# Kernel tuning notes

Measured on AMD Instinct MI355X. Metric: run time of the kernel, lower is better.

The kernel has to match this reference:

```python
import jax, jax.numpy as jnp
import numpy as np

BLOCK_SIZE = 128  # config.block_size; first query block skips intra-block causal mask (faithful to source)
NEG = -1e9       # the module uses -1e9, not -inf, for masking and m_i init


def setup_inputs() -> dict:
    key = jax.random.key(0)
    kq, kk, kv, km = jax.random.split(key, 4)
    B, S, H, D = 2, 2048, 16, 64
    q = jax.random.normal(kq, (B, S, H, D), dtype=jnp.float32)
    k = jax.random.normal(kk, (B, S, H, D), dtype=jnp.float32)
    v = jax.random.normal(kv, (B, S, H, D), dtype=jnp.float32)
    mask = jax.random.randint(km, (B, S), 0, 2).astype(bool)
    mask = mask.at[:, 0].set(True)  # keep first key attendable
    return {"q": q, "k": k, "v": v, "mask": mask}


def reference(q, k, v, mask):
    # q,k,v: [B,S,H,D]; mask: [B,S] bool (True = attend)
    B, S, H, D = q.shape
    scale = 1.0 / np.sqrt(D)
    # config.normalize_query=True -> F.normalize(q, dim=-1) (eps=1e-12)
    qn = q / jnp.maximum(jnp.linalg.norm(q, axis=-1, keepdims=True), 1e-12)
    # scores: [B,S(query),H,S(key)]
    scores = jnp.einsum('bshd,bkhd->bshk', qn, k) * scale
    qi = jnp.arange(S)[:, None]
    ki = jnp.arange(S)[None, :]
    # Faithful causal structure of the blocked PyTorch fallback:
    #  - keys limited to k <= q (triu(diagonal=block_start+1) masking)
    #  - EXCEPT the first query block (block_start==0), where the intra-block
    #    causal mask is skipped (keys still limited to the first block).
    allowed = (ki <= qi) | ((qi < BLOCK_SIZE) & (ki < BLOCK_SIZE))  # [S,S]
    scores = jnp.where(allowed[None, :, None, :], scores, NEG)
    scores = jnp.where(mask[:, None, None, :], scores, NEG)
    p = jax.nn.softmax(scores, axis=-1)
    out = jnp.einsum('bshk,bkhd->bshd', p, v)
    return out
```

## Files before the change

kernel.cpp:

```cpp
#include <hip/hip_runtime.h>
#include <stdint.h>

typedef __attribute__((ext_vector_type(8))) short short8;
typedef __attribute__((ext_vector_type(4))) float floatx4;
typedef __attribute__((ext_vector_type(4))) unsigned int uintx4;
typedef __attribute__((ext_vector_type(2))) unsigned int uintx2;

#define S_LEN 2048
#define NHEAD 16
#define DHEAD 64
#define KB    64
#define KPL   131072
#define VPL   262144
#define VOFF  (32 * KPL)
#define MOFF  (VOFF + 32 * VPL)
#define POFF  (MOFF + 8192)
#define DOFF  (POFF + 512 * 32768)
#define WS_NEEDED ((size_t)DOFF + 512 * 512)
#define NEGINF (-__builtin_inff())
#define LOG2E 1.4426950408889634f
#define CSC   0.011271055f

#define GLOAD_LDS16(gp, lp) \
    __builtin_amdgcn_global_load_lds((const __attribute__((address_space(1))) unsigned int*)(gp), \
                                     (__attribute__((address_space(3))) unsigned int*)(lp), 16, 0, 0)

static __device__ __forceinline__ unsigned f2bf(float f) {
    union { float f; unsigned u; } w; w.f = f;
    return (w.u + 0x7FFFu + ((w.u >> 16) & 1u)) >> 16;
}
static __device__ __forceinline__ unsigned cvtpk(float lo, float hi) {
    unsigned r;
    asm("v_cvt_pk_bf16_f32 %0, %1, %2" : "=v"(r) : "v"(lo), "v"(hi));
    return r;
}
template <int HI>
static __device__ __forceinline__ int cvtfp8(float a, float b, int old) {
    return __builtin_amdgcn_cvt_pk_fp8_f32(a, b, old, HI);
}
static __device__ __forceinline__ floatx4 mfma16(short8 a, short8 b, floatx4 c) {
    return __builtin_amdgcn_mfma_f32_16x16x32_bf16(a, b, c, 0, 0, 0);
}
static __device__ __forceinline__ floatx4 mfma8(long a, long b, floatx4 c) {
    return __builtin_amdgcn_mfma_f32_16x16x32_fp8_fp8(a, b, c, 0, 0, 0);
}

__global__ __launch_bounds__(256) void prep_kernel(
    const float* __restrict__ kg, const float* __restrict__ vg,
    const int* __restrict__ mg, char* __restrict__ ws)
{
    __shared__ unsigned short Tl[64 * 72];
    const int bid = blockIdx.x;
    const int t   = bid & 31;
    const int bh  = bid >> 5;
    const int b   = bh >> 4, h = bh & 15;
    const int tid = threadIdx.x;
    char* kpre = ws + (size_t)bh * KPL;
    char* vpre = ws + VOFF + (size_t)bh * VPL;

    {
        const int r  = tid >> 2;
        const int c4 = tid & 3;
        const size_t grow = (((size_t)b * S_LEN + t * 64 + r) * NHEAD + h) * DHEAD + 16 * c4;
        floatx4 f0 = *(const floatx4*)(kg + grow);
        floatx4 f1 = *(const floatx4*)(kg + grow + 4);
        floatx4 f2 = *(const floatx4*)(kg + grow + 8);
        floatx4 f3 = *(const floatx4*)(kg + grow + 12);
        int w0 = 0, w1 = 0, w2 = 0, w3 = 0;
        w0 = cvtfp8<0>(f0[0], f0[1], w0); w0 = cvtfp8<1>(f0[2], f0[3], w0);
        w1 = cvtfp8<0>(f1[0], f1[1], w1); w1 = cvtfp8<1>(f1[2], f1[3], w1);
        w2 = cvtfp8<0>(f2[0], f2[1], w2); w2 = cvtfp8<1>(f2[2], f2[3], w2);
        w3 = cvtfp8<0>(f3[0], f3[1], w3); w3 = cvtfp8<1>(f3[2], f3[3], w3);
        const int Xr = r & 7;
        char* dst = kpre + t * 4096 + r * 64 + 8 * (((2 * c4) ^ Xr) & ~1);
        *(uintx4*)dst = (Xr & 1)
            ? (uintx4){(unsigned)w2, (unsigned)w3, (unsigned)w0, (unsigned)w1}
            : (uintx4){(unsigned)w0, (unsigned)w1, (unsigned)w2, (unsigned)w3};
    }
    {
        const int key = tid >> 2;
        const int d0  = (tid & 3) * 16;
        const float vz = mg[(size_t)b * S_LEN + t * 64 + key] ? 1.f : 0.f;
        const size_t grow = (((size_t)b * S_LEN + t * 64 + key) * NHEAD + h) * DHEAD;
        #pragma unroll
        for (int q = 0; q < 4; ++q) {
            floatx4 f = *(const floatx4*)(vg + grow + d0 + 4 * q);
            #pragma unroll
            for (int ii = 0; ii < 4; ++ii)
                Tl[(d0 + 4 * q + ii) * 72 + key] = (unsigned short)f2bf(f[ii] * vz);
        }
    }
    __syncthreads();
    {
        const int d  = tid >> 2;
        const int c0 = (tid & 3) * 32;
        const int Xv = (d & 7) << 4;
        #pragma unroll
        for (int cc = 0; cc < 2; ++cc) {
            const int c   = c0 + 16 * cc;
            const int pp0 = (c ^ Xv) >> 1;
            const int blk = pp0 >> 5;
            const int a   = (pp0 & 31) >> 3;
            unsigned short vals[8];
            #pragma unroll
            for (int i = 0; i < 8; ++i) {
                const int key = 32 * blk + ((i < 4) ? (4 * a + i) : (16 + 4 * a + i - 4));
                vals[i] = Tl[d * 72 + key];
            }
            *(uintx4*)(vpre + t * 8192 + d * 128 + c) = *(const uintx4*)vals;
        }
    }
    if (h == 0 && tid < 64) {
        const int key = tid;
        const int gg = (key >> 2) & 3, lo = key & 3;
        const int ks = key >> 5,      hi = (key >> 4) & 1;
        const unsigned short mv = mg[(size_t)b * S_LEN + t * 64 + key] ? 0x3F80 : 0;
        *(unsigned short*)(ws + MOFF + (size_t)b * 4096 + t * 128
                           + gg * 32 + ks * 16 + (4 * hi + lo) * 2) = mv;
    }
}

__global__ __launch_bounds__(512, 4) void fa3_main(
    const float* __restrict__ qg, char* __restrict__ ws,
    float* __restrict__ og)
{
    __shared__ char smem[32768];
    char* Qs  = smem;
    char* KsB = smem + 8192;
    char* VsB = smem + 16384;

    const int tid  = threadIdx.x;
    const int bid  = blockIdx.x;
    const int gidx = bid >> 5;
    const int bh   = bid & 31;
    int qb, chunk; bool split;
    if (gidx < 16) { qb = 15 - (gidx >> 1); chunk = gidx & 1; split = true; }
    else           { qb = 7 - (gidx - 16);  chunk = 0;        split = false; }
    const int b    = bh >> 4;
    const int h    = bh & 15;
    const int w    = tid >> 6;
    const int lane = tid & 63;
    const int g    = lane >> 4;
    const int lm   = lane & 15;
    const int kh   = w >> 2;
    const int wq   = w & 3;
    const char* kpre = ws + (size_t)bh * KPL;
    const char* vpre = ws + VOFF + (size_t)bh * VPL;
    const char* mgf  = ws + MOFF + (size_t)b * 4096;
    const int nkt = (qb == 0) ? 2 : (2 * qb + 2);
    int kt0 = 0, kt1 = nkt;
    if (split) { const int hh = nkt >> 1; kt0 = chunk ? hh : 0; kt1 = chunk ? nkt : hh; }

    if (tid < 256) GLOAD_LDS16(kpre + (size_t)kt0 * 4096 + tid * 16, KsB + tid * 16);
    GLOAD_LDS16(vpre + (size_t)kt0 * 8192 + tid * 16, VsB + tid * 16);

    {
        const int r  = tid >> 2;
        const int q0 = tid & 3;
        const float* src = qg + (((size_t)b * S_LEN + (size_t)qb * 128 + r) * NHEAD + h) * DHEAD + q0 * 16;
        floatx4 f0 = *(const floatx4*)(src + 0);
        floatx4 f1 = *(const floatx4*)(src + 4);
        floatx4 f2 = *(const floatx4*)(src + 8);
        floatx4 f3 = *(const floatx4*)(src + 12);
        float ssq = 0.f;
        #pragma unroll
        for (int i = 0; i < 4; ++i)
            ssq += f0[i]*f0[i] + f1[i]*f1[i] + f2[i]*f2[i] + f3[i]*f3[i];
        ssq += __shfl_xor(ssq, 1);
        ssq += __shfl_xor(ssq, 2);
        const float sc = 16.0f / fmaxf(sqrtf(ssq), 1e-12f);
        int w0 = 0, w1 = 0, w2 = 0, w3 = 0;
        w0 = cvtfp8<0>(f0[0]*sc, f0[1]*sc, w0); w0 = cvtfp8<1>(f0[2]*sc, f0[3]*sc, w0);
        w1 = cvtfp8<0>(f1[0]*sc, f1[1]*sc, w1); w1 = cvtfp8<1>(f1[2]*sc, f1[3]*sc, w1);
        w2 = cvtfp8<0>(f2[0]*sc, f2[1]*sc, w2); w2 = cvtfp8<1>(f2[2]*sc, f2[3]*sc, w2);
        w3 = cvtfp8<0>(f3[0]*sc, f3[1]*sc, w3); w3 = cvtfp8<1>(f3[2]*sc, f3[3]*sc, w3);
        const int Xr = r & 7;
        char* qp = Qs + r * 64 + 8 * (((2 * q0) ^ Xr) & ~1);
        *(uintx4*)qp = (Xr & 1)
            ? (uintx4){(unsigned)w2, (unsigned)w3, (unsigned)w0, (unsigned)w1}
            : (uintx4){(unsigned)w0, (unsigned)w1, (unsigned)w2, (unsigned)w3};
    }
    asm volatile("s_waitcnt vmcnt(0)" ::: "memory");
    __syncthreads();

    const int Xl8  = (lm & 7) << 3;
    const int Xl16 = (lm & 7) << 4;
    long qf8[2][2];
    #pragma unroll
    for (int grp = 0; grp < 2; ++grp) {
        const char* base = Qs + (wq * 32 + grp * 16 + lm) * 64;
        #pragma unroll
        for (int ksd = 0; ksd < 2; ++ksd)
            qf8[grp][ksd] = *(const long*)(base + ((32 * ksd + 8 * g) ^ Xl8));
    }

    floatx4 oacc[2][4];
    floatx4 dacc[2];
    #pragma unroll
    for (int grp = 0; grp < 2; ++grp) {
        dacc[grp] = (floatx4){0.f,0.f,0.f,0.f};
        #pragma unroll
        for (int nt = 0; nt < 4; ++nt) oacc[grp][nt] = (floatx4){0.f,0.f,0.f,0.f};
    }
    floatx4 ZERO4 = (floatx4){0.f,0.f,0.f,0.f};
    asm volatile("" : "+v"(ZERO4));
    const int qgl0 = qb * 128 + wq * 32 + lm;

    int cur = 0;
    for (int kt = kt0; kt < kt1; ++kt) {
        if (kt + 1 < kt1) {
            if (tid < 256)
                GLOAD_LDS16(kpre + (size_t)(kt + 1) * 4096 + tid * 16,
                            KsB + (cur ^ 1) * 4096 + tid * 16);
            GLOAD_LDS16(vpre + (size_t)(kt + 1) * 8192 + tid * 16,
                        VsB + (cur ^ 1) * 8192 + tid * 16);
        }
        const short8 mf = *(const short8*)(mgf + kt * 128 + g * 32 + kh * 16);

        floatx4 st[2][2];
        const char* kbase = KsB + cur * 4096 + kh * 2048 + lm * 64;
        __builtin_amdgcn_s_setprio(1);
        #pragma unroll
        for (int mt = 0; mt < 2; ++mt) {
            long kf = *(const long*)(kbase + mt * 1024 + ((8 * g) ^ Xl8));
            st[0][mt] = mfma8(kf, qf8[0][0], ZERO4);
            st[1][mt] = mfma8(kf, qf8[1][0], ZERO4);
        }
        #pragma unroll
        for (int mt = 0; mt < 2; ++mt) {
            long kf = *(const long*)(kbase + mt * 1024 + ((32 + 8 * g) ^ Xl8));
            st[0][mt] = mfma8(kf, qf8[0][1], st[0][mt]);
            st[1][mt] = mfma8(kf, qf8[1][1], st[1][mt]);
        }
        __builtin_amdgcn_s_setprio(0);

        if ((qb >= 1) && (kt >= 2 * qb)) {
            #pragma unroll
            for (int mt = 0; mt < 2; ++mt)
                #pragma unroll
                for (int j = 0; j < 4; ++j) {
                    const int kgl = kt * KB + kh * 32 + mt * 16 + 4 * g + j;
                    if (kgl > qgl0)      st[0][mt][j] = -1e6f;
                    if (kgl > qgl0 + 16) st[1][mt][j] = -1e6f;
                }
        }

        short8 pa[2];
        #pragma unroll
        for (int grp = 0; grp < 2; ++grp) {
            float p[8];
            #pragma unroll
            for (int mt = 0; mt < 2; ++mt)
                #pragma unroll
                for (int j = 0; j < 4; ++j)
                    p[mt * 4 + j] = exp2f(fmaf(st[grp][mt][j], CSC, -8.0f));
            union { short8 s; uintx4 u; } pu;
            pu.u = (uintx4){ cvtpk(p[0], p[1]), cvtpk(p[2], p[3]),
                             cvtpk(p[4], p[5]), cvtpk(p[6], p[7]) };
            pa[grp] = pu.s;
        }
        __builtin_amdgcn_s_setprio(1);
        dacc[0] = mfma16(pa[0], mf, dacc[0]);
        dacc[1] = mfma16(pa[1], mf, dacc[1]);
        {
            const char* vbase = VsB + cur * 8192 + lm * 128;
            #pragma unroll
            for (int nt = 0; nt < 4; ++nt) {
                short8 vf = *(const short8*)(vbase + nt * 2048 + ((64 * kh + 16 * g) ^ Xl16));
                oacc[0][nt] = mfma16(pa[0], vf, oacc[0][nt]);
                oacc[1][nt] = mfma16(pa[1], vf, oacc[1][nt]);
            }
        }
        __builtin_amdgcn_s_setprio(0);

        asm volatile("s_waitcnt vmcnt(0)" ::: "memory");
        __syncthreads();
        cur ^= 1;
    }

    floatx4* rbuf = (floatx4*)smem;
    float*   dbuf = (float*)smem;
    if (kh == 1) {
        #pragma unroll
        for (int grp = 0; grp < 2; ++grp)
            #pragma unroll
            for (int nt = 0; nt < 4; ++nt)
                rbuf[((grp * 4 + nt) * 4 + wq) * 64 + lane] = oacc[grp][nt];
    }
    __syncthreads();
    if (kh == 0) {
        #pragma unroll
        for (int grp = 0; grp < 2; ++grp)
            #pragma unroll
            for (int nt = 0; nt < 4; ++nt)
                oacc[grp][nt] += rbuf[((grp * 4 + nt) * 4 + wq) * 64 + lane];
    }
    __syncthreads();
    if (kh == 1 && lm == 0) {
        #pragma unroll
        for (int grp = 0; grp < 2; ++grp)
            #pragma unroll
            for (int j = 0; j < 4; ++j)
                dbuf[wq * 32 + grp * 16 + 4 * g + j] = dacc[grp][j];
    }
    __syncthreads();
    if (kh == 0) {
        if (!split) {
            #pragma unroll
            for (int grp = 0; grp < 2; ++grp)
                #pragma unroll
                for (int j = 0; j < 4; ++j) {
                    const int rl = wq * 32 + grp * 16 + 4 * g + j;
                    const float invj = 1.0f / (dacc[grp][j] + dbuf[rl]);
                    float* dst = og + (((size_t)b * S_LEN + qb * 128 + rl) * NHEAD + h) * DHEAD + lm;
                    #pragma unroll
                    for (int nt = 0; nt < 4; ++nt) dst[nt * 16] = oacc[grp][nt][j] * invj;
                }
        } else {
            const int s = ((qb - 8) * 32 + bh) * 2 + chunk;
            float* po = (float*)(ws + POFF + (size_t)s * 32768);
            float* pd = (float*)(ws + DOFF + (size_t)s * 512);
            #pragma unroll
            for (int grp = 0; grp < 2; ++grp)
                #pragma unroll
                for (int j = 0; j < 4; ++j) {
                    const int rl = wq * 32 + grp * 16 + 4 * g + j;
                    #pragma unroll
                    for (int nt = 0; nt < 4; ++nt)
                        po[rl * 64 + nt * 16 + lm] = oacc[grp][nt][j];
                    if (lm == 0) pd[rl] = dacc[grp][j] + dbuf[rl];
                }
        }
    }
}

__global__ __launch_bounds__(256) void fa3_combine(
    const char* __restrict__ ws, float* __restrict__ og)
{
    const int i0  = (blockIdx.x * 256 + threadIdx.x) * 8;
    const int d   = i0 & 63;
    const int row = (i0 >> 6) & 127;
    const int bh  = (i0 >> 13) & 31;
    const int qbi = i0 >> 18;
    const int b   = bh >> 4, h = bh & 15;
    const int s0  = (qbi * 32 + bh) * 2;
    const float* p0 = (const float*)(ws + POFF + (size_t)s0 * 32768) + row * 64 + d;
    const float* p1 = (const float*)(ws + POFF + (size_t)(s0 + 1) * 32768) + row * 64 + d;
    const float den = ((const float*)(ws + DOFF + (size_t)s0 * 512))[row]
                    + ((const float*)(ws + DOFF + (size_t)(s0 + 1) * 512))[row];
    const float inv = 1.0f / den;
    floatx4 a0 = *(const floatx4*)p0, a1 = *(const floatx4*)(p0 + 4);
    floatx4 b0 = *(const floatx4*)p1, b1 = *(const floatx4*)(p1 + 4);
    floatx4 o0, o1;
    #pragma unroll
    for (int i = 0; i < 4; ++i) { o0[i] = (a0[i] + b0[i]) * inv; o1[i] = (a1[i] + b1[i]) * inv; }
    float* dst = og + (((size_t)b * S_LEN + (8 + qbi) * 128 + row) * NHEAD + h) * DHEAD + d;
    *(floatx4*)dst       = o0;
    *(floatx4*)(dst + 4) = o1;
}

__global__ __launch_bounds__(512) void fa3_fallback(
    const float* __restrict__ qg, const float* __restrict__ kg,
    const float* __restrict__ vg, const int* __restrict__ mg,
    float* __restrict__ og)
{
    __shared__ unsigned short Qs[128 * DHEAD];
    __shared__ unsigned short Ks2[KB * DHEAD];
    __shared__ unsigned short Vt[DHEAD * KB];
    __shared__ float Ms[KB];

    const int tid  = threadIdx.x;
    const int bid  = blockIdx.x;
    const int qb   = 15 - (bid >> 5);
    const int bh   = bid & 31;
    const int b    = bh >> 4;
    const int h    = bh & 15;
    const int w    = tid >> 6;
    const int lane = tid & 63;
    const int g    = lane >> 4;
    const int lm   = lane & 15;

    {
        const int r  = tid >> 2;
        const int q0 = tid & 3;
        const float* src = qg + (((size_t)b * S_LEN + (size_t)qb * 128 + r) * NHEAD + h) * DHEAD + q0 * 16;
        floatx4 f0 = *(const floatx4*)(src + 0);
        floatx4 f1 = *(const floatx4*)(src + 4);
        floatx4 f2 = *(const floatx4*)(src + 8);
        floatx4 f3 = *(const floatx4*)(src + 12);
        float ssq = 0.f;
        #pragma unroll
        for (int i = 0; i < 4; ++i)
            ssq += f0[i]*f0[i] + f1[i]*f1[i] + f2[i]*f2[i] + f3[i]*f3[i];
        ssq += __shfl_xor(ssq, 1);
        ssq += __shfl_xor(ssq, 2);
        const float sc = 0.125f / fmaxf(sqrtf(ssq), 1e-12f);
        float fv[16];
        #pragma unroll
        for (int i = 0; i < 4; ++i) { fv[i]=f0[i]; fv[4+i]=f1[i]; fv[8+i]=f2[i]; fv[12+i]=f3[i]; }
        unsigned pk[8];
        #pragma unroll
        for (int i = 0; i < 8; ++i)
            pk[i] = f2bf(fv[2*i]*sc) | (f2bf(fv[2*i+1]*sc) << 16);
        const int X = (r & 7) << 4;
        char* qp = (char*)Qs + r * 128;
        *(uintx4*)(qp + ((32*q0)      ^ X)) = (uintx4){pk[0],pk[1],pk[2],pk[3]};
        *(uintx4*)(qp + ((32*q0 + 16) ^ X)) = (uintx4){pk[4],pk[5],pk[6],pk[7]};
    }
    __syncthreads();

    short8 qf[2];
    {
        const int row = w * 16 + lm;
        const int X = (row & 7) << 4;
        const char* base = (const char*)Qs + row * 128;
        #pragma unroll
        for (int ks = 0; ks < 2; ++ks) {
            union { short8 s; uintx2 u[2]; } u;
            u.u[0] = *(const uintx2*)(base + ((64*ks + 8*g)      ^ X));
            u.u[1] = *(const uintx2*)(base + ((64*ks + 8*g + 32) ^ X));
            qf[ks] = u.s;
        }
    }

    floatx4 oacc[4];
    #pragma unroll
    for (int nt = 0; nt < 4; ++nt) oacc[nt] = (floatx4){0.f,0.f,0.f,0.f};
    float mrun = NEGINF, lrun = 0.f;
    const int q_glob = qb * 128 + w * 16 + lm;
    const int nkt = (qb == 0) ? 2 : (2 * qb + 2);

    for (int kt = 0; kt < nkt; ++kt) {
        const int kb0 = kt * KB;
        {
            const int r = tid >> 3;
            const int o = tid & 7;
            const size_t goff = (((size_t)b * S_LEN + kb0 + r) * NHEAD + h) * DHEAD + o * 8;
            floatx4 a0 = *(const floatx4*)(kg + goff);
            floatx4 a1 = *(const floatx4*)(kg + goff + 4);
            floatx4 c0 = *(const floatx4*)(vg + goff);
            floatx4 c1 = *(const floatx4*)(vg + goff + 4);
            uintx4 kw = (uintx4){ f2bf(a0[0]) | (f2bf(a0[1])<<16),
                                  f2bf(a0[2]) | (f2bf(a0[3])<<16),
                                  f2bf(a1[0]) | (f2bf(a1[1])<<16),
                                  f2bf(a1[2]) | (f2bf(a1[3])<<16) };
            *(uintx4*)((char*)Ks2 + r*128 + ((16*o) ^ ((r & 7) << 4))) = kw;
            float cv[8];
            #pragma unroll
            for (int i = 0; i < 4; ++i) { cv[i] = c0[i]; cv[4+i] = c1[i]; }
            #pragma unroll
            for (int i = 0; i < 8; ++i) {
                const int d = 8*o + i;
                Vt[d*64 + (r ^ (((i ^ o) & 7) << 3))] = (unsigned short)f2bf(cv[i]);
            }
            if (tid < KB) Ms[tid] = mg[(size_t)b * S_LEN + kb0 + tid] ? 0.f : NEGINF;
        }
        __syncthreads();

        floatx4 st[4];
        #pragma unroll
        for (int mt = 0; mt < 4; ++mt) st[mt] = (floatx4){0.f,0.f,0.f,0.f};
        #pragma unroll
        for (int ks = 0; ks < 2; ++ks) {
            #pragma unroll
            for (int mt = 0; mt < 4; ++mt) {
                const int row = mt * 16 + lm;
                const int X = (row & 7) << 4;
                const char* base = (const char*)Ks2 + row * 128;
                union { short8 s; uintx2 u[2]; } u;
                u.u[0] = *(const uintx2*)(base + ((64*ks + 8*g)      ^ X));
                u.u[1] = *(const uintx2*)(base + ((64*ks + 8*g + 32) ^ X));
                st[mt] = mfma16(u.s, qf[ks], st[mt]);
            }
        }

        const bool diag = (qb > 0) && (kt >= 2 * qb);
        float sv[16];
        #pragma unroll
        for (int mt = 0; mt < 4; ++mt) {
            #pragma unroll
            for (int j = 0; j < 4; ++j) {
                const int kl = mt * 16 + 4 * g + j;
                float s = st[mt][j] + Ms[kl];
                if (diag && (kb0 + kl > q_glob)) s = NEGINF;
                sv[mt * 4 + j] = s;
            }
        }

        float rmax = sv[0];
        #pragma unroll
        for (int i = 1; i < 16; ++i) rmax = fmaxf(rmax, sv[i]);
        rmax = fmaxf(rmax, __shfl_xor(rmax, 16));
        rmax = fmaxf(rmax, __shfl_xor(rmax, 32));
        const float mnew = fmaxf(mrun, rmax);
        const float cf = __expf(mrun - mnew);
        float p[16], psum = 0.f;
        #pragma unroll
        for (int i = 0; i < 16; ++i) { p[i] = __expf(sv[i] - mnew); psum += p[i]; }
        psum += __shfl_xor(psum, 16);
        psum += __shfl_xor(psum, 32);
        lrun = lrun * cf + psum;
        mrun = mnew;

        float cj[4];
        #pragma unroll
        for (int j = 0; j < 4; ++j) cj[j] = __shfl(cf, 20 * g + j);
        #pragma unroll
        for (int nt = 0; nt < 4; ++nt)
            #pragma unroll
            for (int j = 0; j < 4; ++j) oacc[nt][j] *= cj[j];

        short8 pa[2];
        #pragma unroll
        for (int ks = 0; ks < 2; ++ks)
            #pragma unroll
            for (int i = 0; i < 8; ++i)
                pa[ks][i] = (short)f2bf(p[(2*ks + (i>>2))*4 + (i&3)]);

        #pragma unroll
        for (int nt = 0; nt < 4; ++nt) {
            const int d = 16 * nt + lm;
            const int xz = (((d & 7) ^ ((d >> 3) & 7)) & 7) << 4;
            const char* vb = (const char*)Vt + d * 128;
            #pragma unroll
            for (int ks = 0; ks < 2; ++ks) {
                union { short8 s; uintx2 u[2]; } vu;
                vu.u[0] = *(const uintx2*)(vb + ((64*ks + 8*g)      ^ xz));
                vu.u[1] = *(const uintx2*)(vb + ((64*ks + 8*g + 32) ^ xz));
                oacc[nt] = mfma16(pa[ks], vu.s, oacc[nt]);
            }
        }
        __syncthreads();
    }

    const float inv = 1.0f / lrun;
    #pragma unroll
    for (int j = 0; j < 4; ++j) {
        const float invj = __shfl(inv, 20 * g + j);
        const int row = qb * 128 + w * 16 + 4 * g + j;
        float* dst = og + (((size_t)b * S_LEN + row) * NHEAD + h) * DHEAD + lm;
        #pragma unroll
        for (int nt = 0; nt < 4; ++nt) dst[nt * 16] = oacc[nt][j] * invj;
    }
}

extern "C" void kernel_launch(void* const* d_in, const int* in_sizes, int n_in,
                              void* d_out, int out_size, void* d_ws, size_t ws_size,
                              hipStream_t stream)
{
    const float* q = (const float*)d_in[0];
    const float* k = (const float*)d_in[1];
    const float* v = (const float*)d_in[2];
    const int*   m = (const int*)d_in[3];
    float* out = (float*)d_out;
    (void)in_sizes; (void)n_in; (void)out_size;
    if (ws_size >= WS_NEEDED) {
        prep_kernel<<<dim3(1024), dim3(256), 0, stream>>>(k, v, m, (char*)d_ws);
        fa3_main<<<dim3(768), dim3(512), 0, stream>>>(q, (char*)d_ws, out);
        fa3_combine<<<dim3(1024), dim3(256), 0, stream>>>((const char*)d_ws, out);
    } else {
        fa3_fallback<<<dim3(512), dim3(512), 0, stream>>>(q, k, v, m, out);
    }
}
```

Before: 56.17 us.

## Prepack K/V in MFMA fragment order and load directly from global, dropping LDS staging

```diff
diff --git a/kernel.cpp b/kernel.cpp
--- a/kernel.cpp
+++ b/kernel.cpp
@@ -5,6 +5,7 @@
 typedef __attribute__((ext_vector_type(4))) float floatx4;
 typedef __attribute__((ext_vector_type(4))) unsigned int uintx4;
 typedef __attribute__((ext_vector_type(2))) unsigned int uintx2;
+typedef unsigned long long ulong64;
 
 #define S_LEN 2048
 #define NHEAD 16
@@ -18,12 +19,7 @@
 #define DOFF  (POFF + 512 * 32768)
 #define WS_NEEDED ((size_t)DOFF + 512 * 512)
 #define NEGINF (-__builtin_inff())
-#define LOG2E 1.4426950408889634f
 #define CSC   0.011271055f
-
-#define GLOAD_LDS16(gp, lp) \
-    __builtin_amdgcn_global_load_lds((const __attribute__((address_space(1))) unsigned int*)(gp), \
-                                     (__attribute__((address_space(3))) unsigned int*)(lp), 16, 0, 0)
 
 static __device__ __forceinline__ unsigned f2bf(float f) {
     union { float f; unsigned u; } w; w.f = f;
@@ -58,24 +54,22 @@
     char* kpre = ws + (size_t)bh * KPL;
     char* vpre = ws + VOFF + (size_t)bh * VPL;
 
-    {
-        const int r  = tid >> 2;
-        const int c4 = tid & 3;
-        const size_t grow = (((size_t)b * S_LEN + t * 64 + r) * NHEAD + h) * DHEAD + 16 * c4;
-        floatx4 f0 = *(const floatx4*)(kg + grow);
-        floatx4 f1 = *(const floatx4*)(kg + grow + 4);
-        floatx4 f2 = *(const floatx4*)(kg + grow + 8);
-        floatx4 f3 = *(const floatx4*)(kg + grow + 12);
-        int w0 = 0, w1 = 0, w2 = 0, w3 = 0;
+    #pragma unroll
+    for (int r2 = 0; r2 < 2; ++r2) {
+        const int ss  = tid + r2 * 256;
+        const int khs = ss >> 8;
+        const int mt  = (ss >> 7) & 1;
+        const int ksd = (ss >> 6) & 1;
+        const int ln  = ss & 63;
+        const int key = khs * 32 + mt * 16 + (ln & 15);
+        const int d0  = 32 * ksd + 8 * (ln >> 4);
+        const float* kr = kg + (((size_t)b * S_LEN + t * 64 + key) * NHEAD + h) * DHEAD + d0;
+        floatx4 f0 = *(const floatx4*)(kr);
+        floatx4 f1 = *(const floatx4*)(kr + 4);
+        int w0 = 0, w1 = 0;
         w0 = cvtfp8<0>(f0[0], f0[1], w0); w0 = cvtfp8<1>(f0[2], f0[3], w0);
         w1 = cvtfp8<0>(f1[0], f1[1], w1); w1 = cvtfp8<1>(f1[2], f1[3], w1);
-        w2 = cvtfp8<0>(f2[0], f2[1], w2); w2 = cvtfp8<1>(f2[2], f2[3], w2);
-        w3 = cvtfp8<0>(f3[0], f3[1], w3); w3 = cvtfp8<1>(f3[2], f3[3], w3);
-        const int Xr = r & 7;
-        char* dst = kpre + t * 4096 + r * 64 + 8 * (((2 * c4) ^ Xr) & ~1);
-        *(uintx4*)dst = (Xr & 1)
-            ? (uintx4){(unsigned)w2, (unsigned)w3, (unsigned)w0, (unsigned)w1}
-            : (uintx4){(unsigned)w0, (unsigned)w1, (unsigned)w2, (unsigned)w3};
+        *(uintx2*)(kpre + t * 4096 + ss * 8) = (uintx2){(unsigned)w0, (unsigned)w1};
     }
     {
         const int key = tid >> 2;
@@ -91,24 +85,24 @@
         }
     }
     __syncthreads();
-    {
-        const int d  = tid >> 2;
-        const int c0 = (tid & 3) * 32;
-        const int Xv = (d & 7) << 4;
-        #pragma unroll
-        for (int cc = 0; cc < 2; ++cc) {
-            const int c   = c0 + 16 * cc;
-            const int pp0 = (c ^ Xv) >> 1;
-            const int blk = pp0 >> 5;
-            const int a   = (pp0 & 31) >> 3;
-            unsigned short vals[8];
-            #pragma unroll
-            for (int i = 0; i < 8; ++i) {
-                const int key = 32 * blk + ((i < 4) ? (4 * a + i) : (16 + 4 * a + i - 4));
-                vals[i] = Tl[d * 72 + key];
-            }
-            *(uintx4*)(vpre + t * 8192 + d * 128 + c) = *(const uintx4*)vals;
-        }
+    #pragma unroll
+    for (int r2 = 0; r2 < 2; ++r2) {
+        const int ss  = tid + r2 * 256;
+        const int khs = ss >> 8;
+        const int nt  = (ss >> 6) & 3;
+        const int ln  = ss & 63;
+        const int d   = 16 * nt + (ln & 15);
+        const int pg  = 4 * khs + (ln >> 4);
+        unsigned short vals[8];
+        #pragma unroll
+        for (int i = 0; i < 8; ++i) {
+            const int p   = pg * 8 + i;
+            const int blk = p >> 5;
+            const int a   = (p >> 3) & 3;
+            const int key = 32 * blk + ((i < 4) ? (4 * a + i) : (16 + 4 * a + i - 4));
+            vals[i] = Tl[d * 72 + key];
+        }
+        *(uintx4*)(vpre + t * 8192 + ss * 16) = *(const uintx4*)vals;
     }
     if (h == 0 && tid < 64) {
         const int key = tid;
@@ -125,9 +119,7 @@
     float* __restrict__ og)
 {
     __shared__ char smem[32768];
-    char* Qs  = smem;
-    char* KsB = smem + 8192;
-    char* VsB = smem + 16384;
+    char* Qs = smem;
 
     const int tid  = threadIdx.x;
     const int bid  = blockIdx.x;
@@ -144,15 +136,9 @@
     const int lm   = lane & 15;
     const int kh   = w >> 2;
     const int wq   = w & 3;
-    const char* kpre = ws + (size_t)bh * KPL;
-    const char* vpre = ws + VOFF + (size_t)bh * VPL;
-    const char* mgf  = ws + MOFF + (size_t)b * 4096;
     const int nkt = (qb == 0) ? 2 : (2 * qb + 2);
     int kt0 = 0, kt1 = nkt;
     if (split) { const int hh = nkt >> 1; kt0 = chunk ? hh : 0; kt1 = chunk ? nkt : hh; }
-
-    if (tid < 256) GLOAD_LDS16(kpre + (size_t)kt0 * 4096 + tid * 16, KsB + tid * 16);
-    GLOAD_LDS16(vpre + (size_t)kt0 * 8192 + tid * 16, VsB + tid * 16);
 
     {
         const int r  = tid >> 2;
@@ -180,11 +166,9 @@
             ? (uintx4){(unsigned)w2, (unsigned)w3, (unsigned)w0, (unsigned)w1}
             : (uintx4){(unsigned)w0, (unsigned)w1, (unsigned)w2, (unsigned)w3};
     }
-    asm volatile("s_waitcnt vmcnt(0)" ::: "memory");
-    __syncthreads();
-
-    const int Xl8  = (lm & 7) << 3;
-    const int Xl16 = (lm & 7) << 4;
+    __syncthreads();
+
+    const int Xl8 = (lm & 7) << 3;
     long qf8[2][2];
     #pragma unroll
     for (int grp = 0; grp < 2; ++grp) {
@@ -193,6 +177,10 @@
         for (int ksd = 0; ksd < 2; ++ksd)
             qf8[grp][ksd] = *(const long*)(base + ((32 * ksd + 8 * g) ^ Xl8));
     }
+
+    const char* kp = ws + (size_t)bh * KPL + (size_t)kt0 * 4096 + kh * 2048 + lane * 8;
+    const char* vp = ws + VOFF + (size_t)bh * VPL + (size_t)kt0 * 8192 + kh * 4096 + lane * 16;
+    const char* mp = ws + MOFF + (size_t)b * 4096 + (size_t)kt0 * 128 + g * 32 + kh * 16;
 
     floatx4 oacc[2][4];
     floatx4 dacc[2];
@@ -206,32 +194,28 @@
     asm volatile("" : "+v"(ZERO4));
     const int qgl0 = qb * 128 + wq * 32 + lm;
 
-    int cur = 0;
     for (int kt = kt0; kt < kt1; ++kt) {
-        if (kt + 1 < kt1) {
-            if (tid < 256)
-                GLOAD_LDS16(kpre + (size_t)(kt + 1) * 4096 + tid * 16,
-                            KsB + (cur ^ 1) * 4096 + tid * 16);
-            GLOAD_LDS16(vpre + (size_t)(kt + 1) * 8192 + tid * 16,
-                        VsB + (cur ^ 1) * 8192 + tid * 16);
-        }
-        const short8 mf = *(const short8*)(mgf + kt * 128 + g * 32 + kh * 16);
+        const ulong64 k00 = *(const ulong64*)(kp);
+        const ulong64 k01 = *(const ulong64*)(kp + 512);
+        const ulong64 k10 = *(const ulong64*)(kp + 1024);
+        const ulong64 k11 = *(const ulong64*)(kp + 1536);
+        const short8 vf0 = *(const short8*)(vp);
+        const short8 vf1 = *(const short8*)(vp + 1024);
+        const short8 vf2 = *(const short8*)(vp + 2048);
+        const short8 vf3 = *(const short8*)(vp + 3072);
+        const short8 mf  = *(const short8*)(mp);
+        kp += 4096; vp += 8192; mp += 128;
 
         floatx4 st[2][2];
-        const char* kbase = KsB + cur * 4096 + kh * 2048 + lm * 64;
         __builtin_amdgcn_s_setprio(1);
-        #pragma unroll
-        for (int mt = 0; mt < 2; ++mt) {
-            long kf = *(const long*)(kbase + mt * 1024 + ((8 * g) ^ Xl8));
-            st[0][mt] = mfma8(kf, qf8[0][0], ZERO4);
-            st[1][mt] = mfma8(kf, qf8[1][0], ZERO4);
-        }
-        #pragma unroll
-        for (int mt = 0; mt < 2; ++mt) {
-            long kf = *(const long*)(kbase + mt * 1024 + ((32 + 8 * g) ^ Xl8));
-            st[0][mt] = mfma8(kf, qf8[0][1], st[0][mt]);
-            st[1][mt] = mfma8(kf, qf8[1][1], st[1][mt]);
-        }
+        st[0][0] = mfma8((long)k00, qf8[0][0], ZERO4);
+        st[1][0] = mfma8((long)k00, qf8[1][0], ZERO4);
+        st[0][1] = mfma8((long)k10, qf8[0][0], ZERO4);
+        st[1][1] = mfma8((long)k10, qf8[1][0], ZERO4);
+        st[0][0] = mfma8((long)k01, qf8[0][1], st[0][0]);
+        st[1][0] = mfma8((long)k01, qf8[1][1], st[1][0]);
+        st[0][1] = mfma8((long)k11, qf8[0][1], st[0][1]);
+        st[1][1] = mfma8((long)k11, qf8[1][1], st[1][1]);
         __builtin_amdgcn_s_setprio(0);
 
         if ((qb >= 1) && (kt >= 2 * qb)) {
@@ -262,21 +246,17 @@
         __builtin_amdgcn_s_setprio(1);
         dacc[0] = mfma16(pa[0], mf, dacc[0]);
         dacc[1] = mfma16(pa[1], mf, dacc[1]);
-        {
-            const char* vbase = VsB + cur * 8192 + lm * 128;
-            #pragma unroll
-            for (int nt = 0; nt < 4; ++nt) {
-                short8 vf = *(const short8*)(vbase + nt * 2048 + ((64 * kh + 16 * g) ^ Xl16));
-                oacc[0][nt] = mfma16(pa[0], vf, oacc[0][nt]);
-                oacc[1][nt] = mfma16(pa[1], vf, oacc[1][nt]);
-            }
-        }
+        oacc[0][0] = mfma16(pa[0], vf0, oacc[0][0]);
+        oacc[1][0] = mfma16(pa[1], vf0, oacc[1][0]);
+        oacc[0][1] = mfma16(pa[0], vf1, oacc[0][1]);
+        oacc[1][1] = mfma16(pa[1], vf1, oacc[1][1]);
+        oacc[0][2] = mfma16(pa[0], vf2, oacc[0][2]);
+        oacc[1][2] = mfma16(pa[1], vf2, oacc[1][2]);
+        oacc[0][3] = mfma16(pa[0], vf3, oacc[0][3]);
+        oacc[1][3] = mfma16(pa[1], vf3, oacc[1][3]);
         __builtin_amdgcn_s_setprio(0);
-
-        asm volatile("s_waitcnt vmcnt(0)" ::: "memory");
-        __syncthreads();
-        cur ^= 1;
-    }
+    }
+    __syncthreads();
 
     floatx4* rbuf = (floatx4*)smem;
     float*   dbuf = (float*)smem;
```

Measured after the change: 52.88 us. -5.9%, faster.
